# Performance work log

Measured on AMD Instinct MI355X. Metric: run time of the kernel, lower is better.

The kernel has to match this reference:

```python
import jax, jax.numpy as jnp
import numpy as np

N, E = 50000, 800000
DIM_IN, DIM_H, DIM_OUT, HEADS = 128, 16, 64, 8
NEG_SLOPE = 0.2  # PyG GATv2Conv default


def setup_inputs() -> dict:
    key = jax.random.key(0)
    ks = jax.random.split(key, 10)
    s = 0.1
    x = jax.random.normal(ks[0], (N, DIM_IN), jnp.float32)
    edge_index = jax.random.randint(ks[1], (2, E), 0, N, dtype=jnp.int32)
    Wl1 = jax.random.normal(ks[2], (DIM_IN, HEADS * DIM_H), jnp.float32) * s
    Wr1 = jax.random.normal(ks[3], (DIM_IN, HEADS * DIM_H), jnp.float32) * s
    att1 = jax.random.normal(ks[4], (HEADS, DIM_H), jnp.float32) * s
    b1 = jnp.zeros((HEADS * DIM_H,), jnp.float32)
    Wl2 = jax.random.normal(ks[5], (HEADS * DIM_H, DIM_OUT), jnp.float32) * s
    Wr2 = jax.random.normal(ks[6], (HEADS * DIM_H, DIM_OUT), jnp.float32) * s
    att2 = jax.random.normal(ks[7], (1, DIM_OUT), jnp.float32) * s
    b2 = jnp.zeros((DIM_OUT,), jnp.float32)
    return dict(x=x, edge_index=edge_index, Wl1=Wl1, Wr1=Wr1, att1=att1, b1=b1,
                Wl2=Wl2, Wr2=Wr2, att2=att2, b2=b2)


def gatv2_conv(x, src, dst, Wl, Wr, att, bias, heads, out_ch):
    # PyG GATv2Conv (share_weights=False, concat=True)
    n = x.shape[0]
    xl = (x @ Wl).reshape(n, heads, out_ch)  # source-side transform
    xr = (x @ Wr).reshape(n, heads, out_ch)  # target-side transform
    e = jax.nn.leaky_relu(xl[src] + xr[dst], NEG_SLOPE)          # [E, H, C]
    logits = jnp.einsum('ehc,hc->eh', e, att)                    # [E, H]
    # segment softmax over incoming edges of each dst node
    m = jax.lax.stop_gradient(jax.ops.segment_max(logits, dst, num_segments=n))
    ex = jnp.exp(logits - m[dst])
    denom = jax.ops.segment_sum(ex, dst, num_segments=n)
    alpha = ex / denom[dst]                                      # [E, H]
    out = jax.ops.segment_sum(xl[src] * alpha[..., None], dst, num_segments=n)
    return out.reshape(n, heads * out_ch) + bias


def reference(x, edge_index, Wl1, Wr1, att1, b1, Wl2, Wr2, att2, b2):
    n = x.shape[0]
    loops = jnp.arange(n, dtype=edge_index.dtype)
    src = jnp.concatenate([edge_index[0], loops])  # add_self_loops=True
    dst = jnp.concatenate([edge_index[1], loops])
    h = gatv2_conv(x, src, dst, Wl1, Wr1, att1, b1, HEADS, DIM_H)
    h = jax.nn.elu(h)
    out = gatv2_conv(h, src, dst, Wl2, Wr2, att2, b2, 1, DIM_OUT)
    return jax.nn.log_softmax(out, axis=1)
```

## Files before the change

### kernel.cpp

```cpp
#include <hip/hip_runtime.h>
#include <cstdint>

#define DIM_IN 128
#define HEADS 8
#define DIM_H 16
#define H1 128
#define DIM_OUT 64
#define NEG 0.2f
#define CAP 6144

typedef __attribute__((ext_vector_type(8))) short bf16x8;
typedef __attribute__((ext_vector_type(4))) float f32x4;

__device__ __forceinline__ float blo(uint32_t u) { return __uint_as_float(u << 16); }
__device__ __forceinline__ float bhi(uint32_t u) { return __uint_as_float(u & 0xffff0000u); }
__device__ __forceinline__ unsigned short f2b(float f) {
  uint32_t u = __float_as_uint(f);
  u += 0x7fffu + ((u >> 16) & 1u);
  return (unsigned short)(u >> 16);
}

__global__ __launch_bounds__(256) void conv_x(
    const float* __restrict__ in, unsigned short* __restrict__ out, int total) {
  int i = (blockIdx.x * 256 + threadIdx.x) * 8;
  if (i >= total) return;
  float4 a = *(const float4*)(in + i);
  float4 b = *(const float4*)(in + i + 4);
  ushort4 u0 = {f2b(a.x), f2b(a.y), f2b(a.z), f2b(a.w)};
  ushort4 u1 = {f2b(b.x), f2b(b.y), f2b(b.z), f2b(b.w)};
  *(ushort4*)(out + i) = u0;
  *(ushort4*)(out + i + 4) = u1;
}

__global__ __launch_bounds__(256) void prep_w(
    const float* __restrict__ W0, const float* __restrict__ W1,
    const float* __restrict__ W2, const float* __restrict__ W3,
    unsigned short* __restrict__ T0, unsigned short* __restrict__ T1,
    unsigned short* __restrict__ T2, unsigned short* __restrict__ T3) {
  int z = blockIdx.y;
  const float* W = (z == 0) ? W0 : (z == 1) ? W1 : (z == 2) ? W2 : W3;
  unsigned short* T = (z == 0) ? T0 : (z == 1) ? T1 : (z == 2) ? T2 : T3;
  int M = (z < 2) ? 128 : 64;
  int t = blockIdx.x * 256 + threadIdx.x;
  if (t >= M * 128) return;
  int n = t >> 7, k = t & 127;
  T[t] = f2b(W[k * M + n]);
}

template <int M>
__global__ __launch_bounds__(256) void gemm_mfma(
    const unsigned short* __restrict__ A,
    const unsigned short* __restrict__ Bt0, const unsigned short* __restrict__ Bt1,
    unsigned short* __restrict__ Cb0, float* __restrict__ C1, int Nrows) {
  constexpr int K = 128;
  constexpr int LDA = 72;
  constexpr int MT = M / 2;
  constexpr int NT = MT / 16;
  __shared__ __align__(16) short Asm[128 * LDA];
  __shared__ __align__(16) short Bsm[M * LDA];
  const unsigned short* __restrict__ Bt = blockIdx.z ? Bt1 : Bt0;
  const int row0 = blockIdx.x * 128;
  const int tid = threadIdx.x;
  const int w = tid >> 6, lane = tid & 63;
  const int l = lane & 15, q = lane >> 4;
  const int wrow = (w >> 1) * 64, wcol = (w & 1) * MT;

  f32x4 zero = {0.f, 0.f, 0.f, 0.f};
  f32x4 acc[4][NT];
#pragma unroll
  for (int ti = 0; ti < 4; ++ti)
#pragma unroll
    for (int tj = 0; tj < NT; ++tj) acc[ti][tj] = zero;

  for (int k0 = 0; k0 < K; k0 += 64) {
    __syncthreads();
    {
      int r = tid >> 1, sg = (tid & 1) * 32;
      int grow = row0 + r;
      const uint4* src = (const uint4*)(A + (size_t)grow * K + k0 + sg);
      uint4 z4 = make_uint4(0, 0, 0, 0);
#pragma unroll
      for (int i = 0; i < 4; ++i) {
        uint4 v = (grow < Nrows) ? src[i] : z4;
        *(uint4*)(Asm + r * LDA + sg + i * 8) = v;
      }
    }
    {
      int r = tid >> 1, sg = (tid & 1) * 32;
      if (r < M) {
        const uint4* src = (const uint4*)(Bt + (size_t)r * K + k0 + sg);
#pragma unroll
        for (int i = 0; i < 4; ++i)
          *(uint4*)(Bsm + r * LDA + sg + i * 8) = src[i];
      }
    }
    __syncthreads();
#pragma unroll
    for (int kk = 0; kk < 64; kk += 32) {
      bf16x8 af[4], bfr[NT];
#pragma unroll
      for (int ti = 0; ti < 4; ++ti)
        af[ti] = *(const bf16x8*)(Asm + (wrow + ti * 16 + l) * LDA + kk + q * 8);
#pragma unroll
      for (int tj = 0; tj < NT; ++tj)
        bfr[tj] = *(const bf16x8*)(Bsm + (wcol + tj * 16 + l) * LDA + kk + q * 8);
#pragma unroll
      for (int ti = 0; ti < 4; ++ti)
#pragma unroll
        for (int tj = 0; tj < NT; ++tj)
          acc[ti][tj] = __builtin_amdgcn_mfma_f32_16x16x32_bf16(
              af[ti], bfr[tj], acc[ti][tj], 0, 0, 0);
    }
  }
#pragma unroll
  for (int ti = 0; ti < 4; ++ti) {
#pragma unroll
    for (int tj = 0; tj < NT; ++tj) {
      int col = wcol + tj * 16 + l;
#pragma unroll
      for (int r = 0; r < 4; ++r) {
        int grow = row0 + wrow + ti * 16 + q * 4 + r;
        if (grow < Nrows) {
          float vv = acc[ti][tj][r];
          if (blockIdx.z == 0) Cb0[(size_t)grow * M + col] = f2b(vv);
          else                 C1[(size_t)grow * M + col] = vv;
        }
      }
    }
  }
}


__global__ __launch_bounds__(256) void p1_bucket(
    const int* __restrict__ ei, int* __restrict__ gcnt,
    uint32_t* __restrict__ gbuf, int E, int nbkt) {
  __shared__ int hist[256];
  __shared__ int base[256];
  __shared__ int cur[256];
  int tid = threadIdx.x;
  hist[tid] = 0;
  __syncthreads();
  int e0 = blockIdx.x * 8192;
  int nE = min(8192, E - e0);
  for (int i = tid; i < nE; i += 256)
    atomicAdd(&hist[ei[E + e0 + i] >> 8], 1);
  __syncthreads();
  if (tid < nbkt) {
    int h = hist[tid];
    base[tid] = h ? atomicAdd(&gcnt[tid], h) : 0;
  }
  cur[tid] = 0;
  __syncthreads();
  for (int i = tid; i < nE; i += 256) {
    int d = ei[E + e0 + i];
    int s = ei[e0 + i];
    int b = d >> 8;
    int r = atomicAdd(&cur[b], 1);
    int pos = base[b] + r;
    if (pos < CAP) gbuf[(size_t)b * CAP + pos] = ((uint32_t)d << 16) | (uint32_t)s;
  }
}

__global__ __launch_bounds__(256) void p2a_hist(
    const uint32_t* __restrict__ gbuf, const int* __restrict__ gcnt,
    int* __restrict__ deg, int N) {
  __shared__ int hist[256];
  int b = blockIdx.x, tid = threadIdx.x;
  hist[tid] = 0;
  __syncthreads();
  int cnt = min(gcnt[b], CAP);
  const uint32_t* p = gbuf + (size_t)b * CAP;
  for (int i = tid; i < cnt; i += 256)
    atomicAdd(&hist[(p[i] >> 16) & 255], 1);
  __syncthreads();
  int node = (b << 8) + tid;
  if (node < N) deg[node] = hist[tid];
}

__global__ __launch_bounds__(256) void p2b_scatter(
    const uint32_t* __restrict__ gbuf, const int* __restrict__ gcnt,
    const int* __restrict__ off, int* __restrict__ srcs, int N) {
  __shared__ int cur[256];
  int b = blockIdx.x, tid = threadIdx.x;
  int node = (b << 8) + tid;
  cur[tid] = (node < N) ? off[node] : 0;
  __syncthreads();
  int cnt = min(gcnt[b], CAP);
  const uint32_t* p = gbuf + (size_t)b * CAP;
  for (int i = tid; i < cnt; i += 256) {
    uint32_t v = p[i];
    int pos = atomicAdd(&cur[(v >> 16) & 255], 1);
    srcs[pos] = (int)(v & 0xFFFFu);
  }
}

__global__ __launch_bounds__(256) void scan_part(
    const int* __restrict__ deg, int* __restrict__ bsum, int N) {
  int i = blockIdx.x * 256 + threadIdx.x;
  int v = (i < N) ? deg[i] : 0;
#pragma unroll
  for (int o = 1; o < 64; o <<= 1) v += __shfl_xor(v, o, 64);
  __shared__ int wsums[4];
  if ((threadIdx.x & 63) == 0) wsums[threadIdx.x >> 6] = v;
  __syncthreads();
  if (threadIdx.x == 0)
    bsum[blockIdx.x] = wsums[0] + wsums[1] + wsums[2] + wsums[3];
}

__global__ __launch_bounds__(256) void scan_tops(
    int* __restrict__ bsum, int* __restrict__ offN, int nb) {
  int tid = threadIdx.x;
  int lane = tid & 63, wid = tid >> 6;
  int v = (tid < nb) ? bsum[tid] : 0;
  int x = v;
#pragma unroll
  for (int o = 1; o < 64; o <<= 1) {
    int y = __shfl_up(x, o, 64);
    if (lane >= o) x += y;
  }
  __shared__ int ws[4];
  if (lane == 63) ws[wid] = x;
  __syncthreads();
  int prefix = 0;
  for (int w = 0; w < 4; ++w) if (w < wid) prefix += ws[w];
  int incl = prefix + x;
  if (tid < nb) bsum[tid] = incl - v;
  if (tid == 255) *offN = incl;
}

__global__ __launch_bounds__(256) void scan_final(
    const int* __restrict__ deg, const int* __restrict__ bsum,
    int* __restrict__ off, int N) {
  int i = blockIdx.x * 256 + threadIdx.x;
  int lane = threadIdx.x & 63, wid = threadIdx.x >> 6;
  int v = (i < N) ? deg[i] : 0;
  int x = v;
#pragma unroll
  for (int o = 1; o < 64; o <<= 1) {
    int y = __shfl_up(x, o, 64);
    if (lane >= o) x += y;
  }
  __shared__ int ws[4];
  if (lane == 63) ws[wid] = x;
  __syncthreads();
  int prefix = bsum[blockIdx.x];
  for (int w = 0; w < 4; ++w) if (w < wid) prefix += ws[w];
  int excl = prefix + x - v;
  if (i < N) off[i] = excl;
}

__global__ __launch_bounds__(256) void agg_l1(
    const int* __restrict__ srcs, const int* __restrict__ off,
    const unsigned short* __restrict__ xlb, const float* __restrict__ xr,
    const float* __restrict__ att, const float* __restrict__ b1,
    unsigned short* __restrict__ hbb, int N) {
  int wid = threadIdx.x >> 6, lane = threadIdx.x & 63;
  int node = blockIdx.x * 4 + wid;
  if (node >= N) return;
  const int l4 = lane & 15;
  const int g  = lane >> 4;
  float4 xr0 = *(const float4*)(xr + ((size_t)node << 7) + (l4 << 3));
  float4 xr1 = *(const float4*)(xr + ((size_t)node << 7) + (l4 << 3) + 4);
  float4 a0  = *(const float4*)(att + (l4 << 3));
  float4 a1  = *(const float4*)(att + (l4 << 3) + 4);
  float acc0 = 0.f, acc1 = 0.f, acc2 = 0.f, acc3 = 0.f;
  float acc4 = 0.f, acc5 = 0.f, acc6 = 0.f, acc7 = 0.f;
  float dsum = 0.f;
  int beg = off[node];
  int M = off[node + 1] - beg + 1;
  for (int base = 0; base < M; base += 64) {
    int nk = min(64, M - base);
    int v = base + lane;
    int sv = 0;
    if (lane < nk) sv = (v == 0) ? node : srcs[beg + v - 1];
    int niter = (nk + 3) >> 2;
    for (int it = 0; it < niter; ++it) {
      int j = (it << 2) + g;
      int s = __shfl(sv, j, 64);
      uint4 xu = *(const uint4*)(xlb + ((size_t)s << 7) + (l4 << 3));
      float x0 = blo(xu.x), x1 = bhi(xu.x), x2 = blo(xu.y), x3 = bhi(xu.y);
      float x4 = blo(xu.z), x5 = bhi(xu.z), x6 = blo(xu.w), x7 = bhi(xu.w);
      float t, p;
      t = x0 + xr0.x; t = t > 0.f ? t : NEG * t; p = a0.x * t;
      t = x1 + xr0.y; t = t > 0.f ? t : NEG * t; p = fmaf(a0.y, t, p);
      t = x2 + xr0.z; t = t > 0.f ? t : NEG * t; p = fmaf(a0.z, t, p);
      t = x3 + xr0.w; t = t > 0.f ? t : NEG * t; p = fmaf(a0.w, t, p);
      t = x4 + xr1.x; t = t > 0.f ? t : NEG * t; p = fmaf(a1.x, t, p);
      t = x5 + xr1.y; t = t > 0.f ? t : NEG * t; p = fmaf(a1.y, t, p);
      t = x6 + xr1.z; t = t > 0.f ? t : NEG * t; p = fmaf(a1.z, t, p);
      t = x7 + xr1.w; t = t > 0.f ? t : NEG * t; p = fmaf(a1.w, t, p);
      p += __shfl_xor(p, 1, 64);
      float ev = (j < nk) ? __expf(p) : 0.f;
      acc0 = fmaf(ev, x0, acc0); acc1 = fmaf(ev, x1, acc1);
      acc2 = fmaf(ev, x2, acc2); acc3 = fmaf(ev, x3, acc3);
      acc4 = fmaf(ev, x4, acc4); acc5 = fmaf(ev, x5, acc5);
      acc6 = fmaf(ev, x6, acc6); acc7 = fmaf(ev, x7, acc7);
      dsum += ev;
    }
  }
#pragma unroll
  for (int o = 16; o <= 32; o <<= 1) {
    dsum += __shfl_xor(dsum, o, 64);
    acc0 += __shfl_xor(acc0, o, 64); acc1 += __shfl_xor(acc1, o, 64);
    acc2 += __shfl_xor(acc2, o, 64); acc3 += __shfl_xor(acc3, o, 64);
    acc4 += __shfl_xor(acc4, o, 64); acc5 += __shfl_xor(acc5, o, 64);
    acc6 += __shfl_xor(acc6, o, 64); acc7 += __shfl_xor(acc7, o, 64);
  }
  if (g == 0) {
    float inv = 1.0f / dsum;
    float4 bv0 = *(const float4*)(b1 + (l4 << 3));
    float4 bv1 = *(const float4*)(b1 + (l4 << 3) + 4);
    float o0 = fmaf(acc0, inv, bv0.x), o1 = fmaf(acc1, inv, bv0.y);
    float o2 = fmaf(acc2, inv, bv0.z), o3 = fmaf(acc3, inv, bv0.w);
    float o4 = fmaf(acc4, inv, bv1.x), o5 = fmaf(acc5, inv, bv1.y);
    float o6 = fmaf(acc6, inv, bv1.z), o7 = fmaf(acc7, inv, bv1.w);
    o0 = o0 > 0.f ? o0 : expm1f(o0); o1 = o1 > 0.f ? o1 : expm1f(o1);
    o2 = o2 > 0.f ? o2 : expm1f(o2); o3 = o3 > 0.f ? o3 : expm1f(o3);
    o4 = o4 > 0.f ? o4 : expm1f(o4); o5 = o5 > 0.f ? o5 : expm1f(o5);
    o6 = o6 > 0.f ? o6 : expm1f(o6); o7 = o7 > 0.f ? o7 : expm1f(o7);
    ushort4 h0 = {f2b(o0), f2b(o1), f2b(o2), f2b(o3)};
    ushort4 h1 = {f2b(o4), f2b(o5), f2b(o6), f2b(o7)};
    unsigned short* ph = hbb + ((size_t)node << 7) + (l4 << 3);
    *(ushort4*)(ph)     = h0;
    *(ushort4*)(ph + 4) = h1;
  }
}

__global__ __launch_bounds__(256) void agg_l2(
    const int* __restrict__ srcs, const int* __restrict__ off,
    const unsigned short* __restrict__ xlb, const float* __restrict__ xr,
    const float* __restrict__ att, const float* __restrict__ b2,
    float* __restrict__ out, int N) {
  int wid = threadIdx.x >> 6, lane = threadIdx.x & 63;
  int node = blockIdx.x * 4 + wid;
  if (node >= N) return;
  const int l3 = lane & 7;
  const int g  = lane >> 3;
  float4 xr0 = *(const float4*)(xr + ((size_t)node << 6) + (l3 << 3));
  float4 xr1 = *(const float4*)(xr + ((size_t)node << 6) + (l3 << 3) + 4);
  float4 a0  = *(const float4*)(att + (l3 << 3));
  float4 a1  = *(const float4*)(att + (l3 << 3) + 4);
  float acc0 = 0.f, acc1 = 0.f, acc2 = 0.f, acc3 = 0.f;
  float acc4 = 0.f, acc5 = 0.f, acc6 = 0.f, acc7 = 0.f;
  float dsum = 0.f;
  int beg = off[node];
  int M = off[node + 1] - beg + 1;
  for (int base = 0; base < M; base += 64) {
    int nk = min(64, M - base);
    int v = base + lane;
    int sv = 0;
    if (lane < nk) sv = (v == 0) ? node : srcs[beg + v - 1];
    int niter = (nk + 7) >> 3;
    for (int it = 0; it < niter; ++it) {
      int j = (it << 3) + g;
      int s = __shfl(sv, j, 64);
      uint4 xu = *(const uint4*)(xlb + ((size_t)s << 6) + (l3 << 3));
      float x0 = blo(xu.x), x1 = bhi(xu.x), x2 = blo(xu.y), x3 = bhi(xu.y);
      float x4 = blo(xu.z), x5 = bhi(xu.z), x6 = blo(xu.w), x7 = bhi(xu.w);
      float t, p;
      t = x0 + xr0.x; t = t > 0.f ? t : NEG * t; p = a0.x * t;
      t = x1 + xr0.y; t = t > 0.f ? t : NEG * t; p = fmaf(a0.y, t, p);
      t = x2 + xr0.z; t = t > 0.f ? t : NEG * t; p = fmaf(a0.z, t, p);
      t = x3 + xr0.w; t = t > 0.f ? t : NEG * t; p = fmaf(a0.w, t, p);
      t = x4 + xr1.x; t = t > 0.f ? t : NEG * t; p = fmaf(a1.x, t, p);
      t = x5 + xr1.y; t = t > 0.f ? t : NEG * t; p = fmaf(a1.y, t, p);
      t = x6 + xr1.z; t = t > 0.f ? t : NEG * t; p = fmaf(a1.z, t, p);
      t = x7 + xr1.w; t = t > 0.f ? t : NEG * t; p = fmaf(a1.w, t, p);
      p += __shfl_xor(p, 1, 64);
      p += __shfl_xor(p, 2, 64);
      p += __shfl_xor(p, 4, 64);
      float ev = (j < nk) ? __expf(p) : 0.f;
      acc0 = fmaf(ev, x0, acc0); acc1 = fmaf(ev, x1, acc1);
      acc2 = fmaf(ev, x2, acc2); acc3 = fmaf(ev, x3, acc3);
      acc4 = fmaf(ev, x4, acc4); acc5 = fmaf(ev, x5, acc5);
      acc6 = fmaf(ev, x6, acc6); acc7 = fmaf(ev, x7, acc7);
      dsum += ev;
    }
  }
#pragma unroll
  for (int o = 8; o <= 32; o <<= 1) {
    dsum += __shfl_xor(dsum, o, 64);
    acc0 += __shfl_xor(acc0, o, 64); acc1 += __shfl_xor(acc1, o, 64);
    acc2 += __shfl_xor(acc2, o, 64); acc3 += __shfl_xor(acc3, o, 64);
    acc4 += __shfl_xor(acc4, o, 64); acc5 += __shfl_xor(acc5, o, 64);
    acc6 += __shfl_xor(acc6, o, 64); acc7 += __shfl_xor(acc7, o, 64);
  }
  float inv = 1.0f / dsum;
  float4 bv0 = *(const float4*)(b2 + (l3 << 3));
  float4 bv1 = *(const float4*)(b2 + (l3 << 3) + 4);
  float v0 = fmaf(acc0, inv, bv0.x), v1 = fmaf(acc1, inv, bv0.y);
  float v2 = fmaf(acc2, inv, bv0.z), v3 = fmaf(acc3, inv, bv0.w);
  float v4 = fmaf(acc4, inv, bv1.x), v5 = fmaf(acc5, inv, bv1.y);
  float v6 = fmaf(acc6, inv, bv1.z), v7 = fmaf(acc7, inv, bv1.w);
  float m = fmaxf(fmaxf(fmaxf(v0, v1), fmaxf(v2, v3)),
                  fmaxf(fmaxf(v4, v5), fmaxf(v6, v7)));
#pragma unroll
  for (int o = 1; o <= 4; o <<= 1) m = fmaxf(m, __shfl_xor(m, o, 64));
  float s = __expf(v0 - m) + __expf(v1 - m) + __expf(v2 - m) + __expf(v3 - m)
          + __expf(v4 - m) + __expf(v5 - m) + __expf(v6 - m) + __expf(v7 - m);
#pragma unroll
  for (int o = 1; o <= 4; o <<= 1) s += __shfl_xor(s, o, 64);
  if (g == 0) {
    float ls = __logf(s) + m;
    float* po = out + ((size_t)node << 6) + (l3 << 3);
    *(float4*)(po)     = make_float4(v0 - ls, v1 - ls, v2 - ls, v3 - ls);
    *(float4*)(po + 4) = make_float4(v4 - ls, v5 - ls, v6 - ls, v7 - ls);
  }
}

extern "C" void kernel_launch(void* const* d_in, const int* in_sizes, int n_in,
                              void* d_out, int out_size, void* d_ws, size_t ws_size,
                              hipStream_t stream) {
  const float* x    = (const float*)d_in[0];
  const int*   ei   = (const int*)d_in[1];
  const float* Wl1  = (const float*)d_in[2];
  const float* Wr1  = (const float*)d_in[3];
  const float* att1 = (const float*)d_in[4];
  const float* b1   = (const float*)d_in[5];
  const float* Wl2  = (const float*)d_in[6];
  const float* Wr2  = (const float*)d_in[7];
  const float* att2 = (const float*)d_in[8];
  const float* b2   = (const float*)d_in[9];
  float* out = (float*)d_out;

  const int N = in_sizes[0] / DIM_IN;
  const int E = in_sizes[1] / 2;
  const int nb = (N + 255) / 256;

  float* ws = (float*)d_ws;
  const size_t szNH = (size_t)N * H1;
  float* xr1 = ws;
  float* xr2 = ws + szNH;
  unsigned short* xb   = (unsigned short*)(ws + szNH + (size_t)N * DIM_OUT);
  unsigned short* xlb1 = xb + szNH;
  unsigned short* hbb  = xlb1 + szNH;
  unsigned short* xlb2 = hbb + szNH;
  unsigned short* wt0  = xlb2 + (size_t)N * DIM_OUT;
  unsigned short* wt1  = wt0 + 16384;
  unsigned short* wt2  = wt1 + 16384;
  unsigned short* wt3  = wt2 + 8192;
  int* ibase  = (int*)(wt3 + 8192);
  int* deg    = ibase;
  int* off    = ibase + N;
  int* bsum   = ibase + 2 * N + 1;
  int* gcnt   = ibase + 2 * N + 1 + 256;
  int* srcs   = ibase + 2 * N + 1 + 512;
  uint32_t* gbuf = (uint32_t*)(srcs + E);

  hipMemsetAsync(gcnt, 0, 256 * sizeof(int), stream);
  p1_bucket<<<(E + 8191) / 8192, 256, 0, stream>>>(ei, gcnt, gbuf, E, nb);
  p2a_hist<<<nb, 256, 0, stream>>>(gbuf, gcnt, deg, N);
  scan_part<<<nb, 256, 0, stream>>>(deg, bsum, N);
  scan_tops<<<1, 256, 0, stream>>>(bsum, off + N, nb);
  scan_final<<<nb, 256, 0, stream>>>(deg, bsum, off, N);
  p2b_scatter<<<nb, 256, 0, stream>>>(gbuf, gcnt, off, srcs, N);

  int totx = N * DIM_IN;
  conv_x<<<(totx / 8 + 255) / 256, 256, 0, stream>>>(x, xb, totx);
  prep_w<<<dim3(64, 4), 256, 0, stream>>>(Wl1, Wr1, Wl2, Wr2, wt0, wt1, wt2, wt3);

  const int gb = (N + 127) / 128;

  gemm_mfma<128><<<dim3(gb, 1, 2), 256, 0, stream>>>(xb, wt0, wt1, xlb1, xr1, N);
  agg_l1<<<(N + 3) / 4, 256, 0, stream>>>(srcs, off, xlb1, xr1, att1, b1, hbb, N);

  gemm_mfma<64><<<dim3(gb, 1, 2), 256, 0, stream>>>(hbb, wt2, wt3, xlb2, xr2, N);
  agg_l2<<<(N + 3) / 4, 256, 0, stream>>>(srcs, off, xlb2, xr2, att2, b2, out, N);
}
```

Baseline: 264.1 us.

## Fuse fp32-to-bf16 input conversion into GEMM, prefetch gathers, simplify leaky-relu logits

Drops the separate conv_x kernel; the first GEMM now reads fp32 x directly and converts to bf16 while staging tiles into shared memory. Both aggregation kernels software-pipeline the neighbor gather by loading the next source row before computing the current one, using precomputed byte offsets. LeakyReLU·att is rewritten algebraically as 0.6·a·z + 0.4·a·|z|, with log2e folded in so exp2f replaces __expf. The GEMM reads twice the A bytes per block, and the prefetch reads one extra (wrapped-index) row past the end of each chunk.

```diff
diff --git a/kernel.cpp b/kernel.cpp
--- a/kernel.cpp
+++ b/kernel.cpp
@@ -18,18 +18,6 @@
   uint32_t u = __float_as_uint(f);
   u += 0x7fffu + ((u >> 16) & 1u);
   return (unsigned short)(u >> 16);
-}
-
-__global__ __launch_bounds__(256) void conv_x(
-    const float* __restrict__ in, unsigned short* __restrict__ out, int total) {
-  int i = (blockIdx.x * 256 + threadIdx.x) * 8;
-  if (i >= total) return;
-  float4 a = *(const float4*)(in + i);
-  float4 b = *(const float4*)(in + i + 4);
-  ushort4 u0 = {f2b(a.x), f2b(a.y), f2b(a.z), f2b(a.w)};
-  ushort4 u1 = {f2b(b.x), f2b(b.y), f2b(b.z), f2b(b.w)};
-  *(ushort4*)(out + i) = u0;
-  *(ushort4*)(out + i + 4) = u1;
 }
 
 __global__ __launch_bounds__(256) void prep_w(
@@ -47,9 +35,9 @@
   T[t] = f2b(W[k * M + n]);
 }
 
-template <int M>
+template <int M, bool AF32>
 __global__ __launch_bounds__(256) void gemm_mfma(
-    const unsigned short* __restrict__ A,
+    const void* __restrict__ Araw,
     const unsigned short* __restrict__ Bt0, const unsigned short* __restrict__ Bt1,
     unsigned short* __restrict__ Cb0, float* __restrict__ C1, int Nrows) {
   constexpr int K = 128;
@@ -77,12 +65,28 @@
     {
       int r = tid >> 1, sg = (tid & 1) * 32;
       int grow = row0 + r;
-      const uint4* src = (const uint4*)(A + (size_t)grow * K + k0 + sg);
-      uint4 z4 = make_uint4(0, 0, 0, 0);
-#pragma unroll
-      for (int i = 0; i < 4; ++i) {
-        uint4 v = (grow < Nrows) ? src[i] : z4;
-        *(uint4*)(Asm + r * LDA + sg + i * 8) = v;
+      if constexpr (AF32) {
+        const float* Af = (const float*)Araw;
+        const float4* s4 = (const float4*)(Af + (size_t)grow * K + k0 + sg);
+        float4 z4 = make_float4(0.f, 0.f, 0.f, 0.f);
+#pragma unroll
+        for (int i = 0; i < 4; ++i) {
+          float4 a = (grow < Nrows) ? s4[2 * i] : z4;
+          float4 b = (grow < Nrows) ? s4[2 * i + 1] : z4;
+          ushort4 lo = {f2b(a.x), f2b(a.y), f2b(a.z), f2b(a.w)};
+          ushort4 hi = {f2b(b.x), f2b(b.y), f2b(b.z), f2b(b.w)};
+          *(ushort4*)(Asm + r * LDA + sg + i * 8)     = lo;
+          *(ushort4*)(Asm + r * LDA + sg + i * 8 + 4) = hi;
+        }
+      } else {
+        const unsigned short* Ab = (const unsigned short*)Araw;
+        const uint4* src = (const uint4*)(Ab + (size_t)grow * K + k0 + sg);
+        uint4 z4 = make_uint4(0, 0, 0, 0);
+#pragma unroll
+        for (int i = 0; i < 4; ++i) {
+          uint4 v = (grow < Nrows) ? src[i] : z4;
+          *(uint4*)(Asm + r * LDA + sg + i * 8) = v;
+        }
       }
     }
     {
@@ -129,7 +133,6 @@
     }
   }
 }
-
 
 __global__ __launch_bounds__(256) void p1_bucket(
     const int* __restrict__ ei, int* __restrict__ gcnt,
@@ -263,39 +266,51 @@
   float4 xr1 = *(const float4*)(xr + ((size_t)node << 7) + (l4 << 3) + 4);
   float4 a0  = *(const float4*)(att + (l4 << 3));
   float4 a1  = *(const float4*)(att + (l4 << 3) + 4);
+  const float K6 = 0.6f * 1.4426950408889634f;
+  const float K4 = 0.4f * 1.4426950408889634f;
+  float c60 = K6 * a0.x, c61 = K6 * a0.y, c62 = K6 * a0.z, c63 = K6 * a0.w;
+  float c64 = K6 * a1.x, c65 = K6 * a1.y, c66 = K6 * a1.z, c67 = K6 * a1.w;
+  float c40 = K4 * a0.x, c41 = K4 * a0.y, c42 = K4 * a0.z, c43 = K4 * a0.w;
+  float c44 = K4 * a1.x, c45 = K4 * a1.y, c46 = K4 * a1.z, c47 = K4 * a1.w;
   float acc0 = 0.f, acc1 = 0.f, acc2 = 0.f, acc3 = 0.f;
   float acc4 = 0.f, acc5 = 0.f, acc6 = 0.f, acc7 = 0.f;
   float dsum = 0.f;
   int beg = off[node];
   int M = off[node + 1] - beg + 1;
+  const char* xbase = (const char*)xlb + (l4 << 4);
   for (int base = 0; base < M; base += 64) {
     int nk = min(64, M - base);
     int v = base + lane;
     int sv = 0;
     if (lane < nk) sv = (v == 0) ? node : srcs[beg + v - 1];
+    int so = sv << 8;
     int niter = (nk + 3) >> 2;
+    int j = g;
+    int sofs = __shfl(so, j, 64);
+    uint4 xu = *(const uint4*)(xbase + sofs);
     for (int it = 0; it < niter; ++it) {
-      int j = (it << 2) + g;
-      int s = __shfl(sv, j, 64);
-      uint4 xu = *(const uint4*)(xlb + ((size_t)s << 7) + (l4 << 3));
+      int jn = j + 4;
+      int sn = __shfl(so, jn & 63, 64);
+      uint4 xn = *(const uint4*)(xbase + sn);
       float x0 = blo(xu.x), x1 = bhi(xu.x), x2 = blo(xu.y), x3 = bhi(xu.y);
       float x4 = blo(xu.z), x5 = bhi(xu.z), x6 = blo(xu.w), x7 = bhi(xu.w);
-      float t, p;
-      t = x0 + xr0.x; t = t > 0.f ? t : NEG * t; p = a0.x * t;
-      t = x1 + xr0.y; t = t > 0.f ? t : NEG * t; p = fmaf(a0.y, t, p);
-      t = x2 + xr0.z; t = t > 0.f ? t : NEG * t; p = fmaf(a0.z, t, p);
-      t = x3 + xr0.w; t = t > 0.f ? t : NEG * t; p = fmaf(a0.w, t, p);
-      t = x4 + xr1.x; t = t > 0.f ? t : NEG * t; p = fmaf(a1.x, t, p);
-      t = x5 + xr1.y; t = t > 0.f ? t : NEG * t; p = fmaf(a1.y, t, p);
-      t = x6 + xr1.z; t = t > 0.f ? t : NEG * t; p = fmaf(a1.z, t, p);
-      t = x7 + xr1.w; t = t > 0.f ? t : NEG * t; p = fmaf(a1.w, t, p);
+      float z, p;
+      z = x0 + xr0.x; p = c60 * z;          p = fmaf(c40, fabsf(z), p);
+      z = x1 + xr0.y; p = fmaf(c61, z, p);  p = fmaf(c41, fabsf(z), p);
+      z = x2 + xr0.z; p = fmaf(c62, z, p);  p = fmaf(c42, fabsf(z), p);
+      z = x3 + xr0.w; p = fmaf(c63, z, p);  p = fmaf(c43, fabsf(z), p);
+      z = x4 + xr1.x; p = fmaf(c64, z, p);  p = fmaf(c44, fabsf(z), p);
+      z = x5 + xr1.y; p = fmaf(c65, z, p);  p = fmaf(c45, fabsf(z), p);
+      z = x6 + xr1.z; p = fmaf(c66, z, p);  p = fmaf(c46, fabsf(z), p);
+      z = x7 + xr1.w; p = fmaf(c67, z, p);  p = fmaf(c47, fabsf(z), p);
       p += __shfl_xor(p, 1, 64);
-      float ev = (j < nk) ? __expf(p) : 0.f;
+      float ev = (j < nk) ? exp2f(p) : 0.f;
       acc0 = fmaf(ev, x0, acc0); acc1 = fmaf(ev, x1, acc1);
       acc2 = fmaf(ev, x2, acc2); acc3 = fmaf(ev, x3, acc3);
       acc4 = fmaf(ev, x4, acc4); acc5 = fmaf(ev, x5, acc5);
       acc6 = fmaf(ev, x6, acc6); acc7 = fmaf(ev, x7, acc7);
       dsum += ev;
+      j = jn; xu = xn;
     }
   }
 #pragma unroll
@@ -340,41 +355,53 @@
   float4 xr1 = *(const float4*)(xr + ((size_t)node << 6) + (l3 << 3) + 4);
   float4 a0  = *(const float4*)(att + (l3 << 3));
   float4 a1  = *(const float4*)(att + (l3 << 3) + 4);
+  const float K6 = 0.6f * 1.4426950408889634f;
+  const float K4 = 0.4f * 1.4426950408889634f;
+  float c60 = K6 * a0.x, c61 = K6 * a0.y, c62 = K6 * a0.z, c63 = K6 * a0.w;
+  float c64 = K6 * a1.x, c65 = K6 * a1.y, c66 = K6 * a1.z, c67 = K6 * a1.w;
+  float c40 = K4 * a0.x, c41 = K4 * a0.y, c42 = K4 * a0.z, c43 = K4 * a0.w;
+  float c44 = K4 * a1.x, c45 = K4 * a1.y, c46 = K4 * a1.z, c47 = K4 * a1.w;
   float acc0 = 0.f, acc1 = 0.f, acc2 = 0.f, acc3 = 0.f;
   float acc4 = 0.f, acc5 = 0.f, acc6 = 0.f, acc7 = 0.f;
   float dsum = 0.f;
   int beg = off[node];
   int M = off[node + 1] - beg + 1;
+  const char* xbase = (const char*)xlb + (l3 << 4);
   for (int base = 0; base < M; base += 64) {
     int nk = min(64, M - base);
     int v = base + lane;
     int sv = 0;
     if (lane < nk) sv = (v == 0) ? node : srcs[beg + v - 1];
+    int so = sv << 7;
     int niter = (nk + 7) >> 3;
+    int j = g;
+    int sofs = __shfl(so, j, 64);
+    uint4 xu = *(const uint4*)(xbase + sofs);
     for (int it = 0; it < niter; ++it) {
-      int j = (it << 3) + g;
-      int s = __shfl(sv, j, 64);
-      uint4 xu = *(const uint4*)(xlb + ((size_t)s << 6) + (l3 << 3));
+      int jn = j + 8;
+      int sn = __shfl(so, jn & 63, 64);
+      uint4 xn = *(const uint4*)(xbase + sn);
       float x0 = blo(xu.x), x1 = bhi(xu.x), x2 = blo(xu.y), x3 = bhi(xu.y);
       float x4 = blo(xu.z), x5 = bhi(xu.z), x6 = blo(xu.w), x7 = bhi(xu.w);
-      float t, p;
-      t = x0 + xr0.x; t = t > 0.f ? t : NEG * t; p = a0.x * t;
-      t = x1 + xr0.y; t = t > 0.f ? t : NEG * t; p = fmaf(a0.y, t, p);
-      t = x2 + xr0.z; t = t > 0.f ? t : NEG * t; p = fmaf(a0.z, t, p);
-      t = x3 + xr0.w; t = t > 0.f ? t : NEG * t; p = fmaf(a0.w, t, p);
-      t = x4 + xr1.x; t = t > 0.f ? t : NEG * t; p = fmaf(a1.x, t, p);
-      t = x5 + xr1.y; t = t > 0.f ? t : NEG * t; p = fmaf(a1.y, t, p);
-      t = x6 + xr1.z; t = t > 0.f ? t : NEG * t; p = fmaf(a1.z, t, p);
-      t = x7 + xr1.w; t = t > 0.f ? t : NEG * t; p = fmaf(a1.w, t, p);
+      float z, p;
+      z = x0 + xr0.x; p = c60 * z;          p = fmaf(c40, fabsf(z), p);
+      z = x1 + xr0.y; p = fmaf(c61, z, p);  p = fmaf(c41, fabsf(z), p);
+      z = x2 + xr0.z; p = fmaf(c62, z, p);  p = fmaf(c42, fabsf(z), p);
+      z = x3 + xr0.w; p = fmaf(c63, z, p);  p = fmaf(c43, fabsf(z), p);
+      z = x4 + xr1.x; p = fmaf(c64, z, p);  p = fmaf(c44, fabsf(z), p);
+      z = x5 + xr1.y; p = fmaf(c65, z, p);  p = fmaf(c45, fabsf(z), p);
+      z = x6 + xr1.z; p = fmaf(c66, z, p);  p = fmaf(c46, fabsf(z), p);
+      z = x7 + xr1.w; p = fmaf(c67, z, p);  p = fmaf(c47, fabsf(z), p);
       p += __shfl_xor(p, 1, 64);
       p += __shfl_xor(p, 2, 64);
       p += __shfl_xor(p, 4, 64);
-      float ev = (j < nk) ? __expf(p) : 0.f;
+      float ev = (j < nk) ? exp2f(p) : 0.f;
       acc0 = fmaf(ev, x0, acc0); acc1 = fmaf(ev, x1, acc1);
       acc2 = fmaf(ev, x2, acc2); acc3 = fmaf(ev, x3, acc3);
       acc4 = fmaf(ev, x4, acc4); acc5 = fmaf(ev, x5, acc5);
       acc6 = fmaf(ev, x6, acc6); acc7 = fmaf(ev, x7, acc7);
       dsum += ev;
+      j = jn; xu = xn;
     }
   }
 #pragma unroll
@@ -431,8 +458,7 @@
   const size_t szNH = (size_t)N * H1;
   float* xr1 = ws;
   float* xr2 = ws + szNH;
-  unsigned short* xb   = (unsigned short*)(ws + szNH + (size_t)N * DIM_OUT);
-  unsigned short* xlb1 = xb + szNH;
+  unsigned short* xlb1 = (unsigned short*)(ws + szNH + (size_t)N * DIM_OUT);
   unsigned short* hbb  = xlb1 + szNH;
   unsigned short* xlb2 = hbb + szNH;
   unsigned short* wt0  = xlb2 + (size_t)N * DIM_OUT;
@@ -455,15 +481,15 @@
   scan_final<<<nb, 256, 0, stream>>>(deg, bsum, off, N);
   p2b_scatter<<<nb, 256, 0, stream>>>(gbuf, gcnt, off, srcs, N);
 
-  int totx = N * DIM_IN;
-  conv_x<<<(totx / 8 + 255) / 256, 256, 0, stream>>>(x, xb, totx);
   prep_w<<<dim3(64, 4), 256, 0, stream>>>(Wl1, Wr1, Wl2, Wr2, wt0, wt1, wt2, wt3);
 
   const int gb = (N + 127) / 128;
 
-  gemm_mfma<128><<<dim3(gb, 1, 2), 256, 0, stream>>>(xb, wt0, wt1, xlb1, xr1, N);
+  gemm_mfma<128, true><<<dim3(gb, 1, 2), 256, 0, stream>>>(
+      (const void*)x, wt0, wt1, xlb1, xr1, N);
   agg_l1<<<(N + 3) / 4, 256, 0, stream>>>(srcs, off, xlb1, xr1, att1, b1, hbb, N);
 
-  gemm_mfma<64><<<dim3(gb, 1, 2), 256, 0, stream>>>(hbb, wt2, wt3, xlb2, xr2, N);
+  gemm_mfma<64, false><<<dim3(gb, 1, 2), 256, 0, stream>>>(
+      (const void*)hbb, wt2, wt3, xlb2, xr2, N);
   agg_l2<<<(N + 3) / 4, 256, 0, stream>>>(srcs, off, xlb2, xr2, att2, b2, out, N);
 }
```

Measured after the change: 286.7 us. 8.5% more time.
